# Optimization experiments

Hardware: AMD Instinct MI355X
Metric: run time of the kernel (lower is better)

## Reference

```python
import jax, jax.numpy as jnp
import numpy as np

B, S, D = 2, 2048, 1024
H, KVH = 16, 4
HD = D // H          # 64
REP = H // KVH       # 4
ROPE_THETA = 10000.0


def setup_inputs() -> dict:
    key = jax.random.key(0)
    ks = jax.random.split(key, 6)
    x = jax.random.normal(ks[0], (B, S, D), dtype=jnp.float32)
    sc = 0.02
    wq = jax.random.normal(ks[1], (D, H * HD), dtype=jnp.float32) * sc
    wk = jax.random.normal(ks[2], (D, KVH * HD), dtype=jnp.float32) * sc
    wv = jax.random.normal(ks[3], (D, KVH * HD), dtype=jnp.float32) * sc
    wo = jax.random.normal(ks[4], (H * HD, D), dtype=jnp.float32) * sc
    # Llama-style rotary frequencies: freqs_cis[t, j] = exp(i * t * theta^{-2j/hd})
    inv_freq = 1.0 / (ROPE_THETA ** (jnp.arange(0, HD, 2, dtype=jnp.float32) / HD))  # [HD/2]
    t = jnp.arange(S, dtype=jnp.float32)
    ang = jnp.outer(t, inv_freq)                     # [S, HD/2]
    freqs_cos = jnp.cos(ang)
    freqs_sin = jnp.sin(ang)
    # additive causal mask [1,1,S,S]
    neg = jnp.float32(-1e9)
    mask = jnp.where(jnp.tril(jnp.ones((S, S), dtype=bool)), 0.0, neg)[None, None]
    return {"x": x, "wq": wq, "wk": wk, "wv": wv, "wo": wo,
            "freqs_cos": freqs_cos, "freqs_sin": freqs_sin, "mask": mask}


def _rope(t, cos, sin):
    # t: [B,S,h,HD]; cos/sin: [S,HD/2]; complex rotation on consecutive pairs
    tr = t[..., 0::2]
    ti = t[..., 1::2]
    c = cos[None, :, None, :]
    s = sin[None, :, None, :]
    or_ = tr * c - ti * s
    oi_ = tr * s + ti * c
    return jnp.stack([or_, oi_], axis=-1).reshape(t.shape)


def reference(x, wq, wk, wv, wo, freqs_cos, freqs_sin, mask):
    b, s, _ = x.shape
    xq = (x @ wq).reshape(b, s, H, HD)
    xk = (x @ wk).reshape(b, s, KVH, HD)
    xv = (x @ wv).reshape(b, s, KVH, HD)
    xq = _rope(xq, freqs_cos, freqs_sin)
    xk = _rope(xk, freqs_cos, freqs_sin)
    # repeat_kv: each kv head repeated REP times -> [b,s,H,HD]
    keys = jnp.repeat(xk, REP, axis=2)
    values = jnp.repeat(xv, REP, axis=2)
    q = xq.transpose(0, 2, 1, 3)      # [b,H,s,HD]
    k = keys.transpose(0, 2, 1, 3)
    v = values.transpose(0, 2, 1, 3)
    scores = jnp.einsum('bhqd,bhkd->bhqk', q, k) / jnp.sqrt(jnp.float32(HD))
    scores = scores + mask
    probs = jax.nn.softmax(scores.astype(jnp.float32), axis=-1).astype(q.dtype)
    out = jnp.einsum('bhqk,bhkd->bhqd', probs, v)
    out = out.transpose(0, 2, 1, 3).reshape(b, s, H * HD)
    return out @ wo
```

## Files before the change

### kernel.cpp

```cpp
#include <hip/hip_runtime.h>

typedef short bf8 __attribute__((ext_vector_type(8)));
typedef float f32x4 __attribute__((ext_vector_type(4)));
typedef float f32x16 __attribute__((ext_vector_type(16)));
typedef int i32x4 __attribute__((ext_vector_type(4)));

__device__ __forceinline__ ushort f2b(float f) {
  unsigned x = __builtin_bit_cast(unsigned, f);
  unsigned r = (x + 0x7fffu + ((x >> 16) & 1u)) >> 16;
  return (ushort)r;
}
__device__ __forceinline__ float b2f(ushort u) {
  unsigned x = ((unsigned)u) << 16;
  return __builtin_bit_cast(float, x);
}

__device__ __forceinline__ f32x4 mfma16(bf8 a, bf8 b, f32x4 c) {
  return __builtin_amdgcn_mfma_f32_16x16x32_bf16(a, b, c, 0, 0, 0);
}
__device__ __forceinline__ f32x16 mfma32(bf8 a, bf8 b, f32x16 c) {
  return __builtin_amdgcn_mfma_f32_32x32x16_bf16(a, b, c, 0, 0, 0);
}

__device__ __forceinline__ float fexp2(float x) {
#if __has_builtin(__builtin_amdgcn_exp2f)
  return __builtin_amdgcn_exp2f(x);
#else
  return exp2f(x);
#endif
}

__device__ __forceinline__ uint cvtpk(float lo, float hi_) {
  uint r;
  asm("v_cvt_pk_bf16_f32 %0, %1, %2" : "=v"(r) : "v"(lo), "v"(hi_));
  return r;
}
__device__ __forceinline__ void plswap(uint& a, uint& b) {
  asm("v_permlane32_swap_b32 %0, %1" : "+v"(a), "+v"(b));
}

__device__ __forceinline__ void gload16(const ushort* g, ushort* l) {
  __builtin_amdgcn_global_load_lds(
      (const __attribute__((address_space(1))) void*)g,
      (__attribute__((address_space(3))) void*)l, 16, 0, 0);
}

__global__ __launch_bounds__(256) void prep1(
    const float* __restrict__ x, const float* __restrict__ wq,
    const float* __restrict__ wk, const float* __restrict__ wv,
    const float* __restrict__ wo, ushort* __restrict__ xb,
    ushort* __restrict__ wqkvT, ushort* __restrict__ woT) {
  __shared__ float tile[32][33];
  const int bid = blockIdx.x;
  if (bid < 4096) {
    const int i = (bid * 256 + threadIdx.x) * 4;
    float4 v = *(const float4*)(x + i);
    ushort4 o;
    o.x = f2b(v.x); o.y = f2b(v.y); o.z = f2b(v.z); o.w = f2b(v.w);
    *(ushort4*)(xb + i) = o;
    return;
  }
  int t = bid - 4096;
  const float* src;
  ushort* dst;
  int N;
  if (t < 1024) {
    src = wq; dst = wqkvT; N = 1024;
  } else if (t < 1280) {
    src = wk; dst = wqkvT + 1024 * 1024; N = 256; t -= 1024;
  } else if (t < 1536) {
    src = wv; dst = wqkvT + 1280 * 1024; N = 256; t -= 1280;
  } else {
    src = wo; dst = woT; N = 1024; t -= 1536;
  }
  const int kx = (t & 31) * 32, nx = (t >> 5) * 32;
  const int tx = threadIdx.x & 31, ty = threadIdx.x >> 5;
#pragma unroll
  for (int i = ty; i < 32; i += 8)
    tile[i][tx] = src[(size_t)(kx + i) * N + nx + tx];
  __syncthreads();
#pragma unroll
  for (int i = ty; i < 32; i += 8)
    dst[(size_t)(nx + i) * 1024 + kx + tx] = f2b(tile[tx][i]);
}

template <bool OUT_BF16>
__global__ __launch_bounds__(256) void gemm_bt(const ushort* __restrict__ A,
                                               const ushort* __restrict__ Bt,
                                               void* __restrict__ Cv, int M,
                                               int N, int K, int nbx) {
  __shared__ ushort aL[2][64 * 64];
  __shared__ ushort bL[2][128 * 64];
  const int tid = threadIdx.x;
  const int wid = tid >> 6, lane = tid & 63;
  const int l15 = lane & 15, l4 = lane >> 4;
  const int qch = gridDim.x >> 3;
  const int sw = (blockIdx.x & 7) * qch + (blockIdx.x >> 3);
  const int bxi = sw % nbx, byi = sw / nbx;
  const int bm = byi * 64, bn = bxi * 128;
  const int wr = (wid & 1) * 32, wc = (wid >> 1) * 64;
  const int nIter = K >> 6;

  auto stage = [&](int it, int par) {
    const int kb = it * 64;
#pragma unroll
    for (int i = 0; i < 2; ++i) {
      const int e = (i * 256 + tid) * 8;
      const int r = e >> 6, c = e & 63;
      gload16(A + (size_t)(bm + r) * K + kb + c,
              &aL[par][i * 2048 + wid * 512]);
    }
#pragma unroll
    for (int i = 0; i < 4; ++i) {
      const int e = (i * 256 + tid) * 8;
      const int r = e >> 6, c = e & 63;
      gload16(Bt + (size_t)(bn + r) * K + kb + c,
              &bL[par][i * 2048 + wid * 512]);
    }
  };

  stage(0, 0);
  f32x4 acc[2][4] = {};
  for (int it = 0; it < nIter; ++it) {
    const int par = it & 1;
    asm volatile("s_waitcnt vmcnt(0)" ::: "memory");
    __builtin_amdgcn_s_barrier();
    asm volatile("" ::: "memory");
    if (it + 1 < nIter) stage(it + 1, par ^ 1);
    bf8 af[2][2], bfr[4][2];
#pragma unroll
    for (int i = 0; i < 2; ++i)
#pragma unroll
      for (int kk = 0; kk < 2; ++kk)
        af[i][kk] =
            *(const bf8*)&aL[par][(wr + i * 16 + l15) * 64 + kk * 32 + l4 * 8];
#pragma unroll
    for (int j = 0; j < 4; ++j)
#pragma unroll
      for (int kk = 0; kk < 2; ++kk)
        bfr[j][kk] =
            *(const bf8*)&bL[par][(wc + j * 16 + l15) * 64 + kk * 32 + l4 * 8];
    asm volatile("s_waitcnt lgkmcnt(0)" ::: "memory");
    __builtin_amdgcn_sched_barrier(0);
#pragma unroll
    for (int kk = 0; kk < 2; ++kk)
#pragma unroll
      for (int i = 0; i < 2; ++i)
#pragma unroll
        for (int j = 0; j < 4; ++j)
          acc[i][j] = mfma16(af[i][kk], bfr[j][kk], acc[i][j]);
  }
#pragma unroll
  for (int i = 0; i < 2; ++i)
#pragma unroll
    for (int j = 0; j < 4; ++j)
#pragma unroll
      for (int r = 0; r < 4; ++r) {
        const size_t row = bm + wr + i * 16 + l4 * 4 + r;
        const size_t col = bn + wc + j * 16 + l15;
        if constexpr (OUT_BF16)
          ((ushort*)Cv)[row * N + col] = f2b(acc[i][j][r]);
        else
          ((float*)Cv)[row * N + col] = acc[i][j][r];
      }
}

__global__ __launch_bounds__(256) void prep2(const ushort* __restrict__ qkv,
                                             const float* __restrict__ fc,
                                             const float* __restrict__ fs,
                                             ushort* __restrict__ qh,
                                             ushort* __restrict__ kh,
                                             ushort* __restrict__ vT) {
  __shared__ ushort tile[64][65];
  if (blockIdx.x < 10240) {
    const int idx = blockIdx.x * 256 + threadIdx.x;
    const int u = idx % 640;
    const int m = idx / 640;
    const int s = m & 2047, b = m >> 11;
    int col, j;
    if (u < 512) {
      j = u & 31;
      col = (u >> 5) * 64 + 2 * j;
    } else {
      j = (u - 512) & 31;
      col = 1024 + ((u - 512) >> 5) * 64 + 2 * j;
    }
    const uint pr = *(const uint*)(qkv + (size_t)m * 1536 + col);
    const float tr = b2f((ushort)(pr & 0xffff));
    const float ti = b2f((ushort)(pr >> 16));
    const float c = fc[s * 32 + j], sn = fs[s * 32 + j];
    float orr = tr * c - ti * sn;
    float oi = tr * sn + ti * c;
    if (u < 512) {
      orr *= 0.18033688f;
      oi *= 0.18033688f;
      const uint w = (uint)f2b(orr) | ((uint)f2b(oi) << 16);
      *(uint*)(qh + ((size_t)(b * 16 + (u >> 5)) * 2048 + s) * 64 + 2 * j) = w;
    } else {
      const uint w = (uint)f2b(orr) | ((uint)f2b(oi) << 16);
      const int kv = (u - 512) >> 5;
      *(uint*)(kh + ((size_t)(b * 4 + kv) * 2048 + s) * 64 + 2 * j) = w;
    }
    return;
  }
  const int id = blockIdx.x - 10240;
  const int st = id & 31, kv = (id >> 5) & 3, b = id >> 7;
  const int tid = threadIdx.x;
  for (int e = tid; e < 4096; e += 256) {
    const int r = e >> 6, c = e & 63;
    tile[r][c] =
        qkv[(size_t)(b * 2048 + st * 64 + r) * 1536 + 1280 + kv * 64 + c];
  }
  __syncthreads();
  for (int e = tid; e < 4096; e += 256) {
    const int d = e >> 6, c = e & 63;
    vT[((size_t)(b * 4 + kv) * 64 + d) * 2048 + st * 64 + c] = tile[c][d];
  }
}


#define MCONST 12.0f

__device__ __forceinline__ void astep2(const bf8 (&kfA)[4], const bf8 (&kfB)[4],
                                       const bf8 (&vfA)[4], const bf8 (&vfB)[4],
                                       const bf8 (&qf)[4], f32x16& o0,
                                       f32x16& o1, float& l, int k0, int qg,
                                       bool maskt, int hi) {
  f32x16 s0 = {}, s1 = {};
  __builtin_amdgcn_s_setprio(1);
#pragma unroll
  for (int ks = 0; ks < 4; ++ks) s0 = mfma32(kfA[ks], qf[ks], s0);
#pragma unroll
  for (int ks = 0; ks < 4; ++ks) s1 = mfma32(kfB[ks], qf[ks], s1);
  __builtin_amdgcn_s_setprio(0);
  if (maskt) {
#pragma unroll
    for (int r = 0; r < 16; ++r) {
      const int key = k0 + (r & 3) + 8 * (r >> 2) + 4 * hi;
      if (key > qg) s0[r] = -1e30f;
      if (key + 32 > qg) s1[r] = -1e30f;
    }
  }
  float t[16];
#pragma unroll
  for (int r = 0; r < 16; ++r) {
    s0[r] = fexp2(s0[r] - MCONST);
    s1[r] = fexp2(s1[r] - MCONST);
    t[r] = s0[r] + s1[r];
  }
#pragma unroll
  for (int st = 8; st > 0; st >>= 1)
#pragma unroll
    for (int r = 0; r < st; ++r) t[r] += t[r + st];
  l += t[0] + __shfl_xor(t[0], 32);
  bf8 pa[4];
  {
    uint a0 = cvtpk(s0[0], s0[1]), a1 = cvtpk(s0[2], s0[3]);
    uint b0 = cvtpk(s0[4], s0[5]), b1 = cvtpk(s0[6], s0[7]);
    plswap(a0, b0);
    plswap(a1, b1);
    i32x4 w = {(int)a0, (int)a1, (int)b0, (int)b1};
    pa[0] = __builtin_bit_cast(bf8, w);
    uint c0 = cvtpk(s0[8], s0[9]), c1 = cvtpk(s0[10], s0[11]);
    uint d0 = cvtpk(s0[12], s0[13]), d1 = cvtpk(s0[14], s0[15]);
    plswap(c0, d0);
    plswap(c1, d1);
    i32x4 w2 = {(int)c0, (int)c1, (int)d0, (int)d1};
    pa[1] = __builtin_bit_cast(bf8, w2);
  }
  {
    uint a0 = cvtpk(s1[0], s1[1]), a1 = cvtpk(s1[2], s1[3]);
    uint b0 = cvtpk(s1[4], s1[5]), b1 = cvtpk(s1[6], s1[7]);
    plswap(a0, b0);
    plswap(a1, b1);
    i32x4 w = {(int)a0, (int)a1, (int)b0, (int)b1};
    pa[2] = __builtin_bit_cast(bf8, w);
    uint c0 = cvtpk(s1[8], s1[9]), c1 = cvtpk(s1[10], s1[11]);
    uint d0 = cvtpk(s1[12], s1[13]), d1 = cvtpk(s1[14], s1[15]);
    plswap(c0, d0);
    plswap(c1, d1);
    i32x4 w2 = {(int)c0, (int)c1, (int)d0, (int)d1};
    pa[3] = __builtin_bit_cast(bf8, w2);
  }
  __builtin_amdgcn_s_setprio(1);
#pragma unroll
  for (int ks = 0; ks < 4; ++ks) o0 = mfma32(vfA[ks], pa[ks], o0);
#pragma unroll
  for (int ks = 0; ks < 4; ++ks) o1 = mfma32(vfB[ks], pa[ks], o1);
  __builtin_amdgcn_s_setprio(0);
}

__device__ __forceinline__ void tile_out(ushort* ow, const f32x16& o0,
                                         const f32x16& o1, float l, int b,
                                         int h, int qw, int l31, int hi,
                                         int lane, ushort* ao) {
  const float inv = 1.0f / l;
#pragma unroll
  for (int dt = 0; dt < 2; ++dt)
#pragma unroll
    for (int rq = 0; rq < 4; ++rq) {
      const f32x16& ac = dt ? o1 : o0;
      uint2 w;
      w.x = (uint)f2b(ac[rq * 4 + 0] * inv) |
            ((uint)f2b(ac[rq * 4 + 1] * inv) << 16);
      w.y = (uint)f2b(ac[rq * 4 + 2] * inv) |
            ((uint)f2b(ac[rq * 4 + 3] * inv) << 16);
      const int d = dt * 32 + 8 * rq + 4 * hi;
      *(uint2*)&ow[l31 * 66 + d] = w;
    }
  asm volatile("s_waitcnt lgkmcnt(0)" ::: "memory");
  __builtin_amdgcn_sched_barrier(0);
  const int rrow = lane >> 4;
  const int rcol = (lane & 15) * 4;
  const size_t gbase = ((size_t)b * 2048 + qw) * 1024 + h * 64;
#pragma unroll
  for (int i = 0; i < 8; ++i) {
    const int rw = i * 4 + rrow;
    uint2 v = *(const uint2*)&ow[rw * 66 + rcol];
    *(uint2*)&ao[gbase + (size_t)rw * 1024 + rcol] = v;
  }
}

__global__ __launch_bounds__(256) void attn_fwd(const ushort* __restrict__ qh,
                                                const ushort* __restrict__ kh,
                                                const ushort* __restrict__ vT,
                                                ushort* __restrict__ ao) {
  __shared__ ushort kls[2][4096];
  __shared__ ushort vls[2][4096];
  __shared__ ushort olds[4][2176];
  const int tid = threadIdx.x;
  const int wid = tid >> 6, lane = tid & 63;
  const int l31 = lane & 31, hi = lane >> 5;
  const int gid = blockIdx.x;
  const int bk = gid & 7;
  const int b = bk >> 2, kv = bk & 3;
  const int rest = gid >> 3;
  const int p = rest & 31, half = rest >> 5;
  const int t = half ? (63 - p) : p;
  const int h = kv * 4 + wid;
  const int n = (32 * t + 95) >> 6;
  const int nss = (n + 1) >> 1;
  const int qg = t * 32 + l31;

  const ushort* kbase = kh + (size_t)(b * 4 + kv) * 2048 * 64;
  const ushort* vbase = vT + (size_t)(b * 4 + kv) * 64 * 2048;

  auto stageTile = [&](int j, int hf) {
    const int k0 = j * 64;
#pragma unroll
    for (int jj2 = 0; jj2 < 2; ++jj2) {
      const int jj = wid + jj2 * 4;
      const int i = jj * 64 + lane;
      const int r = i >> 3, s = i & 7;
      const int sw = (s ^ (r & 7)) << 3;
      gload16(kbase + (size_t)(k0 + r) * 64 + sw, kls[hf] + jj * 512);
      gload16(vbase + (size_t)r * 2048 + k0 + sw, vls[hf] + jj * 512);
    }
  };
  auto stageSS = [&](int ss) {
    const int j0 = 2 * ss;
    const int j1 = (2 * ss + 1 < n) ? (2 * ss + 1) : (n - 1);
    stageTile(j0, 0);
    stageTile(j1, 1);
  };

  stageSS(0);

  bf8 qf[4];
  {
    const ushort* qb = qh + ((size_t)(b * 16 + h) * 2048 + qg) * 64 + hi * 8;
#pragma unroll
    for (int ks = 0; ks < 4; ++ks) qf[ks] = *(const bf8*)(qb + ks * 16);
  }

  f32x16 o0 = {}, o1 = {};
  float l = 0.f;
  const int sw0 = l31 & 7;

  for (int ss = 0; ss < nss; ++ss) {
    asm volatile("s_waitcnt vmcnt(0)" ::: "memory");
    __builtin_amdgcn_s_barrier();
    asm volatile("" ::: "memory");
    bf8 kfA[2][4], kfB[2][4], vfA[2][4], vfB[2][4];
#pragma unroll
    for (int hf = 0; hf < 2; ++hf)
#pragma unroll
      for (int ks = 0; ks < 4; ++ks) {
        const int c2 = 2 * ks + hi;
        const int off = (c2 ^ sw0) << 3;
        kfA[hf][ks] = *(const bf8*)&kls[hf][l31 * 64 + off];
        kfB[hf][ks] = *(const bf8*)&kls[hf][(32 + l31) * 64 + off];
        vfA[hf][ks] = *(const bf8*)&vls[hf][l31 * 64 + off];
        vfB[hf][ks] = *(const bf8*)&vls[hf][(32 + l31) * 64 + off];
      }
    asm volatile("s_waitcnt lgkmcnt(0)" ::: "memory");
    __builtin_amdgcn_sched_barrier(0);
    __builtin_amdgcn_s_barrier();
    if (ss + 1 < nss) stageSS(ss + 1);
    const int j0 = 2 * ss, j1 = 2 * ss + 1;
    astep2(kfA[0], kfB[0], vfA[0], vfB[0], qf, o0, o1, l, j0 * 64, qg,
           j0 == n - 1, hi);
    if (j1 < n)
      astep2(kfA[1], kfB[1], vfA[1], vfB[1], qf, o0, o1, l, j1 * 64, qg,
             j1 == n - 1, hi);
  }
  tile_out(olds[wid], o0, o1, l, b, h, t * 32, l31, hi, lane, ao);
}

extern "C" void kernel_launch(void* const* d_in, const int* in_sizes, int n_in,
                              void* d_out, int out_size, void* d_ws,
                              size_t ws_size, hipStream_t stream) {
  (void)in_sizes; (void)n_in; (void)out_size; (void)ws_size;
  const float* x = (const float*)d_in[0];
  const float* wq = (const float*)d_in[1];
  const float* wk = (const float*)d_in[2];
  const float* wv = (const float*)d_in[3];
  const float* wo = (const float*)d_in[4];
  const float* fc = (const float*)d_in[5];
  const float* fs = (const float*)d_in[6];
  float* out = (float*)d_out;

  ushort* xb = (ushort*)d_ws;
  ushort* wqkvT = xb + 4194304;
  ushort* woT = wqkvT + 1572864;
  ushort* qkv = woT + 1048576;
  ushort* qh = qkv + 6291456;
  ushort* kh = qh + 4194304;
  ushort* vTb = kh + 1048576;
  ushort* ao = vTb + 1048576;

  prep1<<<6656, 256, 0, stream>>>(x, wq, wk, wv, wo, xb, wqkvT, woT);
  gemm_bt<true><<<768, 256, 0, stream>>>(xb, wqkvT, qkv, 4096, 1536, 1024, 12);
  prep2<<<10496, 256, 0, stream>>>(qkv, fc, fs, qh, kh, vTb);
  attn_fwd<<<512, 256, 0, stream>>>(qh, kh, vTb, ao);
  gemm_bt<false><<<512, 256, 0, stream>>>(ao, woT, out, 4096, 1024, 1024, 8);
}
```

Before: 102.6 us.

## Fuse RoPE, head reshaping and V transpose into QKV GEMM epilogue

Replaces the bf16 QKV GEMM plus separate prep2 kernel with a single GEMM whose epilogue applies rotary embedding (pairing lanes via shuffle), the Q scale, and head-major scatter for Q/K, and transposes V through LDS into vT. This removes one kernel launch and the write and re-read of the intermediate qkv buffer. The epilogue now does scattered 2-byte stores and per-element cos/sin loads, which may make the GEMM tail slower. It also rotates fp32 accumulators instead of bf16-rounded values.

Result: faster. 98.01 us (-4.5%).

```diff
diff --git a/kernel.cpp b/kernel.cpp
--- a/kernel.cpp
+++ b/kernel.cpp
@@ -82,6 +82,129 @@
 #pragma unroll
   for (int i = ty; i < 32; i += 8)
     dst[(size_t)(nx + i) * 1024 + kx + tx] = f2b(tile[tx][i]);
+}
+
+__global__ __launch_bounds__(256) void gemm_rope(
+    const ushort* __restrict__ A, const ushort* __restrict__ Bt,
+    const float* __restrict__ fc, const float* __restrict__ fs,
+    ushort* __restrict__ qh, ushort* __restrict__ kh,
+    ushort* __restrict__ vT) {
+  __shared__ ushort aL[2][64 * 64];
+  __shared__ ushort bL[2][128 * 64];
+  const int K = 1024;
+  const int tid = threadIdx.x;
+  const int wid = tid >> 6, lane = tid & 63;
+  const int l15 = lane & 15, l4 = lane >> 4;
+  const int qch = gridDim.x >> 3;
+  const int sw = (blockIdx.x & 7) * qch + (blockIdx.x >> 3);
+  const int bxi = sw % 12, byi = sw / 12;
+  const int bm = byi * 64, bn = bxi * 128;
+  const int wr = (wid & 1) * 32, wc = (wid >> 1) * 64;
+  const int nIter = K >> 6;
+
+  auto stage = [&](int it, int par) {
+    const int kb = it * 64;
+#pragma unroll
+    for (int i = 0; i < 2; ++i) {
+      const int e = (i * 256 + tid) * 8;
+      const int r = e >> 6, c = e & 63;
+      gload16(A + (size_t)(bm + r) * K + kb + c,
+              &aL[par][i * 2048 + wid * 512]);
+    }
+#pragma unroll
+    for (int i = 0; i < 4; ++i) {
+      const int e = (i * 256 + tid) * 8;
+      const int r = e >> 6, c = e & 63;
+      gload16(Bt + (size_t)(bn + r) * K + kb + c,
+              &bL[par][i * 2048 + wid * 512]);
+    }
+  };
+
+  stage(0, 0);
+  f32x4 acc[2][4] = {};
+  for (int it = 0; it < nIter; ++it) {
+    const int par = it & 1;
+    asm volatile("s_waitcnt vmcnt(0)" ::: "memory");
+    __builtin_amdgcn_s_barrier();
+    asm volatile("" ::: "memory");
+    if (it + 1 < nIter) stage(it + 1, par ^ 1);
+    bf8 af[2][2], bfr[4][2];
+#pragma unroll
+    for (int i = 0; i < 2; ++i)
+#pragma unroll
+      for (int kk = 0; kk < 2; ++kk)
+        af[i][kk] =
+            *(const bf8*)&aL[par][(wr + i * 16 + l15) * 64 + kk * 32 + l4 * 8];
+#pragma unroll
+    for (int j = 0; j < 4; ++j)
+#pragma unroll
+      for (int kk = 0; kk < 2; ++kk)
+        bfr[j][kk] =
+            *(const bf8*)&bL[par][(wc + j * 16 + l15) * 64 + kk * 32 + l4 * 8];
+    asm volatile("s_waitcnt lgkmcnt(0)" ::: "memory");
+    __builtin_amdgcn_sched_barrier(0);
+#pragma unroll
+    for (int kk = 0; kk < 2; ++kk)
+#pragma unroll
+      for (int i = 0; i < 2; ++i)
+#pragma unroll
+        for (int j = 0; j < 4; ++j)
+          acc[i][j] = mfma16(af[i][kk], bfr[j][kk], acc[i][j]);
+  }
+
+  if (bxi < 10) {
+    const bool isQ = bxi < 8;
+    const float qs = isQ ? 0.18033688f : 1.0f;
+    const int colbase = bn + wc;
+    const int head = isQ ? (colbase >> 6) : ((colbase - 1024) >> 6);
+    const int nh = isQ ? 16 : 4;
+    ushort* outp = isQ ? qh : kh;
+#pragma unroll
+    for (int i = 0; i < 2; ++i)
+#pragma unroll
+      for (int j = 0; j < 4; ++j) {
+        const int d = j * 16 + l15;
+        const int d2 = d >> 1;
+#pragma unroll
+        for (int r = 0; r < 4; ++r) {
+          const int row = bm + wr + i * 16 + l4 * 4 + r;
+          const int s = row & 2047, bb = row >> 11;
+          const float c = fc[s * 32 + d2], sn = fs[s * 32 + d2];
+          const float val = acc[i][j][r];
+          const float par = __shfl_xor(val, 1);
+          float o;
+          if ((l15 & 1) == 0)
+            o = (val * c - par * sn) * qs;
+          else
+            o = (par * sn + val * c) * qs;
+          outp[((size_t)(bb * nh + head) * 2048 + s) * 64 + d] = f2b(o);
+        }
+      }
+  } else {
+    __syncthreads();
+    ushort* ldsT = &bL[0][0];
+#pragma unroll
+    for (int i = 0; i < 2; ++i)
+#pragma unroll
+      for (int j = 0; j < 4; ++j) {
+        const int cl = wc + j * 16 + l15;
+#pragma unroll
+        for (int r = 0; r < 4; ++r) {
+          const int rl = wr + i * 16 + l4 * 4 + r;
+          ldsT[cl * 68 + rl] = f2b(acc[i][j][r]);
+        }
+      }
+    __syncthreads();
+    const int bb = bm >> 11, sbase = bm & 2047;
+    const int dl = tid >> 1, sh = (tid & 1) * 32;
+    const int gcol = bn + dl - 1280;
+    const int kv = gcol >> 6, d = gcol & 63;
+    ushort* dst = vT + ((size_t)(bb * 4 + kv) * 64 + d) * 2048 + sbase + sh;
+    const ushort* srcl = ldsT + dl * 68 + sh;
+#pragma unroll
+    for (int k = 0; k < 8; ++k)
+      *(uint2*)(dst + k * 4) = *(const uint2*)(srcl + k * 4);
+  }
 }
 
 template <bool OUT_BF16>
@@ -164,60 +287,6 @@
           ((float*)Cv)[row * N + col] = acc[i][j][r];
       }
 }
-
-__global__ __launch_bounds__(256) void prep2(const ushort* __restrict__ qkv,
-                                             const float* __restrict__ fc,
-                                             const float* __restrict__ fs,
-                                             ushort* __restrict__ qh,
-                                             ushort* __restrict__ kh,
-                                             ushort* __restrict__ vT) {
-  __shared__ ushort tile[64][65];
-  if (blockIdx.x < 10240) {
-    const int idx = blockIdx.x * 256 + threadIdx.x;
-    const int u = idx % 640;
-    const int m = idx / 640;
-    const int s = m & 2047, b = m >> 11;
-    int col, j;
-    if (u < 512) {
-      j = u & 31;
-      col = (u >> 5) * 64 + 2 * j;
-    } else {
-      j = (u - 512) & 31;
-      col = 1024 + ((u - 512) >> 5) * 64 + 2 * j;
-    }
-    const uint pr = *(const uint*)(qkv + (size_t)m * 1536 + col);
-    const float tr = b2f((ushort)(pr & 0xffff));
-    const float ti = b2f((ushort)(pr >> 16));
-    const float c = fc[s * 32 + j], sn = fs[s * 32 + j];
-    float orr = tr * c - ti * sn;
-    float oi = tr * sn + ti * c;
-    if (u < 512) {
-      orr *= 0.18033688f;
-      oi *= 0.18033688f;
-      const uint w = (uint)f2b(orr) | ((uint)f2b(oi) << 16);
-      *(uint*)(qh + ((size_t)(b * 16 + (u >> 5)) * 2048 + s) * 64 + 2 * j) = w;
-    } else {
-      const uint w = (uint)f2b(orr) | ((uint)f2b(oi) << 16);
-      const int kv = (u - 512) >> 5;
-      *(uint*)(kh + ((size_t)(b * 4 + kv) * 2048 + s) * 64 + 2 * j) = w;
-    }
-    return;
-  }
-  const int id = blockIdx.x - 10240;
-  const int st = id & 31, kv = (id >> 5) & 3, b = id >> 7;
-  const int tid = threadIdx.x;
-  for (int e = tid; e < 4096; e += 256) {
-    const int r = e >> 6, c = e & 63;
-    tile[r][c] =
-        qkv[(size_t)(b * 2048 + st * 64 + r) * 1536 + 1280 + kv * 64 + c];
-  }
-  __syncthreads();
-  for (int e = tid; e < 4096; e += 256) {
-    const int d = e >> 6, c = e & 63;
-    vT[((size_t)(b * 4 + kv) * 64 + d) * 2048 + st * 64 + c] = tile[c][d];
-  }
-}
-
 
 #define MCONST 12.0f
 
@@ -430,8 +499,7 @@
   ushort* ao = vTb + 1048576;
 
   prep1<<<6656, 256, 0, stream>>>(x, wq, wk, wv, wo, xb, wqkvT, woT);
-  gemm_bt<true><<<768, 256, 0, stream>>>(xb, wqkvT, qkv, 4096, 1536, 1024, 12);
-  prep2<<<10496, 256, 0, stream>>>(qkv, fc, fs, qh, kh, vTb);
+  gemm_rope<<<768, 256, 0, stream>>>(xb, wqkvT, fc, fs, qh, kh, vTb);
   attn_fwd<<<512, 256, 0, stream>>>(qh, kh, vTb, ao);
   gemm_bt<false><<<512, 256, 0, stream>>>(ao, woT, out, 4096, 1024, 1024, 8);
 }
```
